# Kernel tuning notes

Measured on AMD Instinct MI355X. Metric: run time of the kernel, lower is better.

The kernel has to match this reference:

```python
import jax, jax.numpy as jnp
import numpy as np

IS, OS, H = 168, 24, 256           # input window, output horizon, state_hsize
TAU, MAXIMUM = 0.1, 1.0            # tau parameter (non-grad) and series maximum
DILS = [[1, 4], [16, 64]]          # ResidualDRNN groups of dilations


def _lstm(x, wih, whh, bih, bhh):
    """Single-layer LSTM over time-major x: (T, B, C). PyTorch gate order i,f,g,o."""
    def step(carry, xt):
        h, c = carry
        g = xt @ wih.T + h @ whh.T + (bih + bhh)
        i, f, gg, o = jnp.split(g, 4, axis=-1)
        c = jax.nn.sigmoid(f) * c + jax.nn.sigmoid(i) * jnp.tanh(gg)
        h = jax.nn.sigmoid(o) * jnp.tanh(c)
        return (h, c), h
    h0 = jnp.zeros((x.shape[1], H), x.dtype)
    _, hs = jax.lax.scan(step, (h0, h0), x)
    return hs


def _dilated_lstm(x, d, p):
    """Standard DRNN layer: pad T to multiple of d, interleave time into batch, run LSTM."""
    T, B, C = x.shape
    n = -(-T // d)
    xp = jnp.pad(x, ((0, n * d - T), (0, 0), (0, 0)))
    hd = _lstm(xp.reshape(n, d * B, C), *p)
    return hd.reshape(n * d, B, H)[:T]


def _forward(train, init_lev_sm, lstm_params, nl_w, nl_b, sc_w, sc_b):
    B, T = train.shape
    a = jax.nn.sigmoid(init_lev_sm[0])            # lev_sms (idxs are all 0 -> same scalar)
    floor = TAU * MAXIMUM                          # tau * maximum
    # --- exponential-smoothing level recurrence (sequential) ---
    lev0 = jnp.maximum(train[:, 0], floor)
    def step(lev, xt):
        new = jnp.maximum(a * xt + (1.0 - a) * lev, floor)
        return new, new
    _, rest = jax.lax.scan(step, lev0, train[:, 1:].T)
    levs = jnp.concatenate([lev0[None], rest], axis=0).T   # [B, T]
    # --- windowed normalization ---
    w_idx = jnp.arange(IS - 1, T)                           # W = T - IS + 1 window ends
    in_win = train[:, (w_idx - IS + 1)[:, None] + jnp.arange(IS)[None, :]]
    in_win = (in_win / levs[:, w_idx][:, :, None]).transpose(1, 0, 2)    # [W, B, IS]
    o_idx = jnp.arange(IS - 1, T - OS)                      # W_out = T - OS - IS + 1
    out_win = train[:, (o_idx + 1)[:, None] + jnp.arange(OS)[None, :]]
    out_win = (out_win / levs[:, o_idx][:, :, None]).transpose(1, 0, 2)  # [W_out, B, OS]
    # --- ResidualDRNN stack on window_input[:-OS] (time-major: windows are the sequence) ---
    x = in_win[:-OS]
    li = 0
    for g, dils in enumerate(DILS):
        residual = x
        h = x
        for d in dils:
            h = _dilated_lstm(h, d, lstm_params[li])
            li += 1
        x = h + residual if g > 0 else h                    # dropout p=0 -> identity
    x = jnp.tanh(x @ nl_w.T + nl_b)                         # add_nl_layer
    pred = x @ sc_w.T + sc_b                                # scoring
    return pred, out_win


def setup_inputs() -> dict:
    key = jax.random.key(0)
    ks = list(jax.random.split(key, 32))
    B, T = 32, 1024
    inp = {
        "train": jax.random.uniform(ks[0], (B, T), jnp.float32, 0.05, 1.0),
        "val": jax.random.uniform(ks[1], (B, T), jnp.float32, 0.05, 1.0),
        "test": jax.random.uniform(ks[2], (B, T), jnp.float32, 0.05, 1.0),
        "idxs": jnp.zeros((B,), jnp.int32),
        "init_lev_sm": jnp.array([0.5], jnp.float32),
    }
    sizes = [IS, H, H, H]  # input feature size of each of the 4 DRNN layers
    k = 3
    s = 1.0 / np.sqrt(H)
    for i, cin in enumerate(sizes):
        inp[f"wih{i}"] = jax.random.uniform(ks[k], (4 * H, cin), jnp.float32, -s, s); k += 1
        inp[f"whh{i}"] = jax.random.uniform(ks[k], (4 * H, H), jnp.float32, -s, s); k += 1
        inp[f"bih{i}"] = jax.random.uniform(ks[k], (4 * H,), jnp.float32, -s, s); k += 1
        inp[f"bhh{i}"] = jax.random.uniform(ks[k], (4 * H,), jnp.float32, -s, s); k += 1
    inp["nl_w"] = jax.random.uniform(ks[k], (H, H), jnp.float32, -s, s); k += 1
    inp["nl_b"] = jnp.zeros((H,), jnp.float32)
    inp["sc_w"] = jax.random.uniform(ks[k], (OS, H), jnp.float32, -s, s); k += 1
    inp["sc_b"] = jnp.zeros((OS,), jnp.float32)
    return inp


def reference(train, val, test, idxs, init_lev_sm,
              wih0, whh0, bih0, bhh0, wih1, whh1, bih1, bhh1,
              wih2, whh2, bih2, bhh2, wih3, whh3, bih3, bhh3,
              nl_w, nl_b, sc_w, sc_b):
    lstm_params = [(wih0, whh0, bih0, bhh0), (wih1, whh1, bih1, bhh1),
                   (wih2, whh2, bih2, bhh2), (wih3, whh3, bih3, bhh3)]
    # training path (validating=False, testing=False): only `train` is used
    return _forward(train, init_lev_sm, lstm_params, nl_w, nl_b, sc_w, sc_b)
```

## Files before the change

kernel.cpp:

```cpp
#include <hip/hip_runtime.h>
#include <hip/hip_fp16.h>
#include <math.h>

#define TT 833
#define GDIM 1024

typedef _Float16 f16x8 __attribute__((ext_vector_type(8)));
typedef float    f32x4 __attribute__((ext_vector_type(4)));

#if __has_builtin(__builtin_amdgcn_rcpf)
__device__ __forceinline__ float frcp(float x){ return __builtin_amdgcn_rcpf(x); }
#else
__device__ __forceinline__ float frcp(float x){ return 1.f/x; }
#endif

#if __has_builtin(__builtin_amdgcn_sdot4)
__device__ __forceinline__ int sdot4(unsigned a, unsigned b, int c){
  return __builtin_amdgcn_sdot4((int)a, (int)b, c, false);
}
#else
__device__ __forceinline__ int sdot4(unsigned a, unsigned b, int c){
  int ai = (int)a, bi = (int)b;
  c += ((ai<<24)>>24)*((bi<<24)>>24);
  c += ((ai<<16)>>24)*((bi<<16)>>24);
  c += ((ai<<8)>>24)*((bi<<8)>>24);
  c += (ai>>24)*(bi>>24);
  return c;
}
#endif

__device__ __forceinline__ void lds_barrier(){
  asm volatile("s_waitcnt lgkmcnt(0)" ::: "memory");
  __builtin_amdgcn_s_barrier();
  __builtin_amdgcn_sched_barrier(0);
}


__global__ void levels_k(const float* __restrict__ train, const float* __restrict__ ism,
                         float* __restrict__ levs){
  int b = threadIdx.x;
  if (b >= 32) return;
  float a = 1.f/(1.f+expf(-ism[0]));
  const float4* tr4 = reinterpret_cast<const float4*>(train + b*1024);
  float4* lv4 = reinterpret_cast<float4*>(levs + b*1024);
  float lev = 0.f;
  for (int i = 0; i < 256; ++i){
    float4 v = tr4[i];
    float4 o;
    if (i == 0) o.x = lev = fmaxf(v.x, 0.1f);
    else        o.x = lev = fmaxf(fmaf(a, v.x, (1.f-a)*lev), 0.1f);
    o.y = lev = fmaxf(fmaf(a, v.y, (1.f-a)*lev), 0.1f);
    o.z = lev = fmaxf(fmaf(a, v.z, (1.f-a)*lev), 0.1f);
    o.w = lev = fmaxf(fmaf(a, v.w, (1.f-a)*lev), 0.1f);
    lv4[i] = o;
  }
}

__global__ void win_x_k(const float* __restrict__ train, const float* __restrict__ levs,
                        __half* __restrict__ x0){
  int idx = blockIdx.x*256 + threadIdx.x;
  int i = idx % 192;
  int r = idx / 192;
  int b = r & 31;
  int t = r >> 5;
  x0[idx] = (i < 168) ? __float2half(train[b*1024 + t + i] / levs[b*1024 + t + 167])
                      : __float2half(0.f);
}

__global__ void win_out_k(const float* __restrict__ train, const float* __restrict__ levs,
                          float* __restrict__ ow){
  int idx = blockIdx.x*256 + threadIdx.x;
  int o = idx % 24;
  int r = idx / 24;
  int b = r & 31;
  int t = r >> 5;
  ow[idx] = train[b*1024 + 168 + t + o] / levs[b*1024 + t + 167];
}

__global__ void permw_k(const float* __restrict__ wih, const float* __restrict__ bih,
                        const float* __restrict__ bhh, __half* __restrict__ wP,
                        float* __restrict__ bP, int K, int Kpad){
  int t = blockIdx.x;
  int g = ((t & 3) << 8) + (t >> 2);
  for (int k = threadIdx.x; k < Kpad; k += 256)
    wP[(size_t)t*Kpad + k] = (k < K) ? __float2half(wih[(size_t)g*K + k]) : __float2half(0.f);
  if (threadIdx.x == 0) bP[t] = bih[g] + bhh[g];
}

__global__ void cvth_k(const float* __restrict__ s, __half* __restrict__ d, int n){
  int i = blockIdx.x*256 + threadIdx.x;
  if (i < n) d[i] = __float2half(s[i]);
}

__global__ void packq_k(const float* __restrict__ w, uint4* __restrict__ wq,
                        float* __restrict__ sc){
  int t = blockIdx.x*256 + threadIdx.x;
  if (t >= 1024) return;
  int g = ((t & 3) << 8) + (t >> 2);
  const float* row = w + (size_t)g*256;
  float amax = 0.f;
  for (int k = 0; k < 256; ++k) amax = fmaxf(amax, fabsf(row[k]));
  amax = fmaxf(amax, 1e-20f);
  float s = amax/127.f, inv = 127.f/amax;
  sc[t] = s;
  for (int k16 = 0; k16 < 16; ++k16){
    union { uint4 u; signed char b[16]; } r;
    #pragma unroll
    for (int j = 0; j < 16; ++j){
      float q = rintf(row[k16*16 + j]*inv);
      q = fminf(fmaxf(q, -127.f), 127.f);
      r.b[j] = (signed char)q;
    }
    wq[(size_t)k16*1024 + t] = r.u;
  }
}

__global__ __launch_bounds__(256) void proj_direct(
    const _Float16* __restrict__ A, const _Float16* __restrict__ W,
    const float* __restrict__ b1,
    void* __restrict__ C, int Mout, int K, int N, int dil, int act, int outHalf)
{
  const int tid = threadIdx.x;
  const int lane = tid & 63;
  const int w = tid >> 6, wr = w >> 1, wc = w & 1;
  const int m0 = blockIdx.y << 7, n0 = blockIdx.x << 7;
  const int kg = lane >> 4, r16 = lane & 15;

  int srow[4];
  #pragma unroll
  for (int mi = 0; mi < 4; ++mi){
    int m = m0 + wr*64 + mi*16 + r16;
    int row;
    if (dil == 0) row = (m < Mout) ? m : -1;
    else {
      int rows = dil << 5;
      int jj = m / rows;
      int q = m - jj*rows;
      int t = jj*dil + (q >> 5);
      row = (t < TT) ? ((t << 5) + (q & 31)) : -1;
    }
    srow[mi] = row;
  }
  const _Float16* wbase[4];
  #pragma unroll
  for (int nj = 0; nj < 4; ++nj)
    wbase[nj] = W + (size_t)(n0 + wc*64 + nj*16 + r16)*K;

  f32x4 acc[4][4];
  #pragma unroll
  for (int i = 0; i < 4; ++i)
    #pragma unroll
    for (int j = 0; j < 4; ++j) acc[i][j] = (f32x4){0.f,0.f,0.f,0.f};

  const int nkt = K >> 5;
  #pragma unroll 2
  for (int kt = 0; kt < nkt; ++kt){
    const int k = (kt << 5) + kg*8;
    f16x8 af[4], bf[4];
    #pragma unroll
    for (int mi = 0; mi < 4; ++mi){
      af[mi] = (f16x8){0,0,0,0,0,0,0,0};
      if (srow[mi] >= 0)
        af[mi] = *reinterpret_cast<const f16x8*>(A + (size_t)srow[mi]*K + k);
    }
    #pragma unroll
    for (int nj = 0; nj < 4; ++nj)
      bf[nj] = *reinterpret_cast<const f16x8*>(wbase[nj] + k);
    #pragma unroll
    for (int mi = 0; mi < 4; ++mi)
      #pragma unroll
      for (int nj = 0; nj < 4; ++nj)
        acc[mi][nj] = __builtin_amdgcn_mfma_f32_16x16x32_f16(af[mi], bf[nj], acc[mi][nj], 0, 0, 0);
  }
  #pragma unroll
  for (int mi = 0; mi < 4; ++mi){
    #pragma unroll
    for (int p = 0; p < 4; ++p){
      int mrow = m0 + wr*64 + mi*16 + (lane >> 4)*4 + p;
      if (mrow >= Mout) continue;
      #pragma unroll
      for (int nj = 0; nj < 4; ++nj){
        int ncol = n0 + wc*64 + nj*16 + (lane & 15);
        float v = acc[mi][nj][p] + b1[ncol];
        if (act) v = tanhf(v);
        if (outHalf) reinterpret_cast<__half*>(C)[(size_t)mrow*N + ncol] = __float2half(v);
        else reinterpret_cast<float*>(C)[(size_t)mrow*N + ncol] = v;
      }
    }
  }
}

template<int NR>
__global__ __launch_bounds__(512, 1) void srecr2_k(
    const uint4* __restrict__ wq, const float* __restrict__ scale,
    const __half* __restrict__ Gin,
    __half* __restrict__ outh, float* __restrict__ outf,
    int nsteps, int d, int rowsTotal)
{
  __shared__ __align__(16) unsigned int hq[2][NR][64];
  const int tid = threadIdx.x;
  const int s = tid & 1;
  const int j = tid >> 1;
  const int q0 = blockIdx.x*NR;
  const float sg0 = scale[2*tid]*(1.f/127.f);
  const float sg1 = scale[2*tid + 1]*(1.f/127.f);
  uint4 w0_[16], w1_[16];
  #pragma unroll
  for (int kk = 0; kk < 16; ++kk){
    w0_[kk] = wq[(size_t)kk*1024 + 2*tid];
    w1_[kk] = wq[(size_t)kk*1024 + 2*tid + 1];
  }
  float c[NR];
  #pragma unroll
  for (int rr = 0; rr < NR; ++rr) c[rr] = 0.f;
  for (int e = tid; e < 2*NR*64; e += 512) (&hq[0][0][0])[e] = 0u;
  __syncthreads();

  for (int step = 0; step < nsteps; ++step){
    const int cur = step & 1;
    const __half2* gbase = reinterpret_cast<const __half2*>(
        Gin + ((size_t)step*rowsTotal + q0)*GDIM);
    #pragma unroll
    for (int rr = 0; rr < NR; ++rr){
      __half2 g2 = gbase[rr*512 + tid];
      float gin0 = __half2float(__low2half(g2));
      float gin1 = __half2float(__high2half(g2));
      int a00 = 0, a01 = 0, a10 = 0, a11 = 0;
      #pragma unroll
      for (int k16 = 0; k16 < 8; ++k16){
        uint4 ha = *reinterpret_cast<const uint4*>(&hq[cur][rr][4*k16]);
        a00 = sdot4(w0_[k16].x, ha.x, a00); a00 = sdot4(w0_[k16].y, ha.y, a00);
        a00 = sdot4(w0_[k16].z, ha.z, a00); a00 = sdot4(w0_[k16].w, ha.w, a00);
        a10 = sdot4(w1_[k16].x, ha.x, a10); a10 = sdot4(w1_[k16].y, ha.y, a10);
        a10 = sdot4(w1_[k16].z, ha.z, a10); a10 = sdot4(w1_[k16].w, ha.w, a10);
        uint4 hb = *reinterpret_cast<const uint4*>(&hq[cur][rr][4*(k16 + 8)]);
        a01 = sdot4(w0_[k16+8].x, hb.x, a01); a01 = sdot4(w0_[k16+8].y, hb.y, a01);
        a01 = sdot4(w0_[k16+8].z, hb.z, a01); a01 = sdot4(w0_[k16+8].w, hb.w, a01);
        a11 = sdot4(w1_[k16+8].x, hb.x, a11); a11 = sdot4(w1_[k16+8].y, hb.y, a11);
        a11 = sdot4(w1_[k16+8].z, hb.z, a11); a11 = sdot4(w1_[k16+8].w, hb.w, a11);
      }
      float p0 = fmaf((float)(a00 + a01), sg0, gin0);
      float p1 = fmaf((float)(a10 + a11), sg1, gin1);
      float px0 = s ? p0 + p0 : p0;
      float t0 = frcp(1.f + __expf(-px0));
      float a0v = s ? fmaf(2.f, t0, -1.f) : t0;
      float a1v = frcp(1.f + __expf(-p1));
      float b0 = __shfl_xor(a0v, 1);
      float b1 = __shfl_xor(a1v, 1);
      float iv = s ? b0 : a0v;
      float fv = s ? b1 : a1v;
      float gv = s ? a0v : b0;
      float ov = s ? a1v : b1;
      float cn = fmaf(fv, c[rr], iv*gv);
      c[rr] = cn;
      if (s == 0){
        float e2 = __expf(-2.f*cn);
        float h = ov*(1.f - e2)*frcp(1.f + e2);
        int qh = (int)rintf(h*127.f);
        reinterpret_cast<signed char*>(&hq[cur^1][rr][0])[j] = (signed char)qh;
        int q = q0 + rr;
        int tg = step*d + (q >> 5);
        if (tg < TT){
          size_t oi = ((size_t)tg*32 + (q & 31))*256 + j;
          outh[oi] = __float2half(h);
          if (outf) outf[oi] = h;
        }
      }
    }
    lds_barrier();
  }
}

template<int NR>
__global__ __launch_bounds__(1024) void srecq_k(
    const uint4* __restrict__ wq, const float* __restrict__ scale,
    const __half* __restrict__ Gin,
    __half* __restrict__ outh, const float* __restrict__ res,
    int nsteps, int d, int rowsTotal)
{
  __shared__ __align__(16) unsigned int hq[2][NR][64];
  const int tid = threadIdx.x;
  const int lane = tid & 63;
  const int base = lane & ~3;
  const int kg = tid & 3;
  const int j = tid >> 2;
  const int q0 = blockIdx.x*NR;
  const float sg = scale[tid]*(1.f/127.f);
  float c[NR];
  #pragma unroll
  for (int rr = 0; rr < NR; ++rr) c[rr] = 0.f;
  for (int e = tid; e < 2*NR*64; e += 1024) (&hq[0][0][0])[e] = 0u;
  __syncthreads();

  for (int step = 0; step < nsteps; ++step){
    const int cur = step & 1;
    float gin[NR];
    const __half* gbase = Gin + ((size_t)step*rowsTotal + q0)*GDIM;
    #pragma unroll
    for (int rr = 0; rr < NR; ++rr) gin[rr] = __half2float(gbase[rr*GDIM + tid]);
    int acc[NR];
    #pragma unroll
    for (int rr = 0; rr < NR; ++rr) acc[rr] = 0;
    #pragma unroll 4
    for (int k16 = 0; k16 < 16; ++k16){
      uint4 w = wq[(size_t)k16*1024 + tid];
      #pragma unroll
      for (int rr = 0; rr < NR; ++rr){
        uint4 h4 = *reinterpret_cast<const uint4*>(&hq[cur][rr][4*k16]);
        acc[rr] = sdot4(w.x, h4.x, acc[rr]);
        acc[rr] = sdot4(w.y, h4.y, acc[rr]);
        acc[rr] = sdot4(w.z, h4.z, acc[rr]);
        acc[rr] = sdot4(w.w, h4.w, acc[rr]);
      }
    }
    #pragma unroll
    for (int rr = 0; rr < NR; ++rr){
      float p = fmaf((float)acc[rr], sg, gin[rr]);
      float px = (kg == 2) ? p + p : p;
      float sv = frcp(1.f + __expf(-px));
      float a = (kg == 2) ? fmaf(2.f, sv, -1.f) : sv;
      float iv = __shfl(a, base + 0);
      float fv = __shfl(a, base + 1);
      float gv = __shfl(a, base + 2);
      float ov = __shfl(a, base + 3);
      float cn = fmaf(fv, c[rr], iv*gv);
      c[rr] = cn;
      float e2 = __expf(-2.f*cn);
      float h = ov*(1.f - e2)*frcp(1.f + e2);
      if (kg == 0){
        int qh = (int)rintf(h*127.f);
        reinterpret_cast<signed char*>(&hq[cur^1][rr][0])[j] = (signed char)qh;
        int q = q0 + rr;
        int tg = step*d + (q >> 5);
        if (tg < TT){
          size_t oi = ((size_t)tg*32 + (q & 31))*256 + j;
          outh[oi] = __float2half(h + res[oi]);
        }
      }
    }
    lds_barrier();
  }
}

__global__ __launch_bounds__(256) void sc_head(const __half* __restrict__ xt, const float* __restrict__ w,
                        const float* __restrict__ bias, float* __restrict__ outp, int M){
  __shared__ float arow[8][256];
  int m0 = blockIdx.x << 3;
  int tid = threadIdx.x;
  #pragma unroll
  for (int i = 0; i < 8; ++i){
    int e = tid + (i << 8);
    int r = e >> 8, k = e & 255;
    arow[r][k] = (m0 + r < M) ? __half2float(xt[(size_t)(m0 + r)*256 + k]) : 0.f;
  }
  __syncthreads();
  int r = tid >> 5, n = tid & 31;
  if (n < 24 && (m0 + r) < M){
    float acc = bias[n];
    const float* wr = w + n*256;
    #pragma unroll 8
    for (int k = 0; k < 256; ++k) acc = fmaf(arow[r][k], wr[k], acc);
    outp[(size_t)(m0 + r)*24 + n] = acc;
  }
}

extern "C" void kernel_launch(void* const* d_in, const int* in_sizes, int n_in,
                              void* d_out, int out_size, void* d_ws, size_t ws_size,
                              hipStream_t stream){
  const float* train = (const float*)d_in[0];
  const float* ism   = (const float*)d_in[4];
  const float* wih[4] = {(const float*)d_in[5], (const float*)d_in[9], (const float*)d_in[13], (const float*)d_in[17]};
  const float* whh[4] = {(const float*)d_in[6], (const float*)d_in[10], (const float*)d_in[14], (const float*)d_in[18]};
  const float* bih[4] = {(const float*)d_in[7], (const float*)d_in[11], (const float*)d_in[15], (const float*)d_in[19]};
  const float* bhh[4] = {(const float*)d_in[8], (const float*)d_in[12], (const float*)d_in[16], (const float*)d_in[20]};
  const float* nl_w = (const float*)d_in[21];
  const float* nl_b = (const float*)d_in[22];
  const float* sc_w = (const float*)d_in[23];
  const float* sc_b = (const float*)d_in[24];
  float* out = (float*)d_out;

  float* ws = (float*)d_ws;
  size_t off = 0;
  float* levs = ws + off;   off += 32768;
  uint4* wqk[4];
  for (int l = 0; l < 4; ++l){ wqk[l] = (uint4*)(ws + off); off += 65536; }
  float* sck[4];
  for (int l = 0; l < 4; ++l){ sck[l] = ws + off; off += 1024; }
  __half* wPh[4];
  for (int l = 0; l < 4; ++l){ wPh[l] = (__half*)(ws + off); off += 131072; }
  float* bP[4];
  for (int l = 0; l < 4; ++l){ bP[l] = ws + off; off += 1024; }
  __half* nlwh = (__half*)(ws + off); off += 32768;
  __half* x0h = (__half*)(ws + off);  off += (size_t)26656*192/2;
  __half* G   = (__half*)(ws + off);  off += (size_t)28672*1024/2;
  __half* h0h = (__half*)(ws + off);  off += (size_t)26656*256/2;
  __half* h1h = (__half*)(ws + off);  off += (size_t)26656*256/2;
  float*  h1f = ws + off;             off += (size_t)26656*256;
  __half* h2h = (__half*)(ws + off);  off += (size_t)26656*256/2;
  __half* xfh = (__half*)(ws + off);  off += (size_t)26656*256/2;
  __half* xth = (__half*)(ws + off);  off += (size_t)26656*256/2;
  (void)ws_size; (void)in_sizes; (void)n_in; (void)out_size;

  levels_k<<<1, 64, 0, stream>>>(train, ism, levs);
  win_x_k<<<19992, 256, 0, stream>>>(train, levs, x0h);
  win_out_k<<<2499, 256, 0, stream>>>(train, levs, out + 639744);
  const int Kin[4]  = {168, 256, 256, 256};
  const int Kpad[4] = {192, 256, 256, 256};
  for (int l = 0; l < 4; ++l){
    packq_k<<<4, 256, 0, stream>>>(whh[l], wqk[l], sck[l]);
    permw_k<<<1024, 256, 0, stream>>>(wih[l], bih[l], bhh[l], wPh[l], bP[l], Kin[l], Kpad[l]);
  }
  cvth_k<<<256, 256, 0, stream>>>(nl_w, nlwh, 65536);

  proj_direct<<<dim3(8,209), 256, 0, stream>>>((const _Float16*)x0h, (const _Float16*)wPh[0], bP[0], G, 26656, 192, 1024, 0, 0, 1);
  srecr2_k<1><<<32, 512, 0, stream>>>(wqk[0], sck[0], G, h0h, nullptr, 833, 1, 32);
  proj_direct<<<dim3(8,209), 256, 0, stream>>>((const _Float16*)h0h, (const _Float16*)wPh[1], bP[1], G, 26752, 256, 1024, 4, 0, 1);
  srecr2_k<1><<<128, 512, 0, stream>>>(wqk[1], sck[1], G, h1h, h1f, 209, 4, 128);
  proj_direct<<<dim3(8,212), 256, 0, stream>>>((const _Float16*)h1h, (const _Float16*)wPh[2], bP[2], G, 27136, 256, 1024, 16, 0, 1);
  srecr2_k<2><<<256, 512, 0, stream>>>(wqk[2], sck[2], G, h2h, nullptr, 53, 16, 512);
  proj_direct<<<dim3(8,224), 256, 0, stream>>>((const _Float16*)h2h, (const _Float16*)wPh[3], bP[3], G, 28672, 256, 1024, 64, 0, 1);
  srecq_k<8><<<256, 1024, 0, stream>>>(wqk[3], sck[3], G, xfh, h1f, 14, 64, 2048);
  proj_direct<<<dim3(2,209), 256, 0, stream>>>((const _Float16*)xfh, (const _Float16*)nlwh, nl_b, xth, 26656, 256, 256, 0, 1, 1);
  sc_head<<<3332, 256, 0, stream>>>(xth, sc_w, sc_b, out, 26656);
}
```

Baseline: 1.761 ms.

## Stage projection GEMM tiles through LDS with 256x128 blocks of 512 threads

The input projection GEMM now stages the A and B tiles into padded shared memory each k-step, with 8 waves per block covering a 256x128 output tile, instead of each wave loading its MFMA fragments straight from global memory. The aim is to share the loaded tiles across waves and use coalesced global loads, which cuts redundant global traffic. In exchange it adds two barriers per k-iteration with no double buffering, and larger blocks, which may limit overlap. An unrelated reorder of two sdot4 calls in the recurrence kernel is also included.

```diff
diff --git a/kernel.cpp b/kernel.cpp
--- a/kernel.cpp
+++ b/kernel.cpp
@@ -115,36 +115,34 @@
   }
 }
 
-__global__ __launch_bounds__(256) void proj_direct(
+__global__ __launch_bounds__(512) void proj_mfma(
     const _Float16* __restrict__ A, const _Float16* __restrict__ W,
     const float* __restrict__ b1,
     void* __restrict__ C, int Mout, int K, int N, int dil, int act, int outHalf)
 {
+  __shared__ _Float16 As[256*40];
+  __shared__ _Float16 Bs[128*40];
   const int tid = threadIdx.x;
   const int lane = tid & 63;
   const int w = tid >> 6, wr = w >> 1, wc = w & 1;
-  const int m0 = blockIdx.y << 7, n0 = blockIdx.x << 7;
-  const int kg = lane >> 4, r16 = lane & 15;
-
-  int srow[4];
-  #pragma unroll
-  for (int mi = 0; mi < 4; ++mi){
-    int m = m0 + wr*64 + mi*16 + r16;
-    int row;
-    if (dil == 0) row = (m < Mout) ? m : -1;
+  const int m0 = blockIdx.y << 8, n0 = blockIdx.x << 7;
+
+  const int rowA = tid >> 1;
+  const int halfsel = tid & 1;
+  int srcrow;
+  {
+    int m = m0 + rowA;
+    if (dil == 0) srcrow = (m < Mout) ? m : -1;
     else {
       int rows = dil << 5;
       int jj = m / rows;
       int q = m - jj*rows;
       int t = jj*dil + (q >> 5);
-      row = (t < TT) ? ((t << 5) + (q & 31)) : -1;
-    }
-    srow[mi] = row;
-  }
-  const _Float16* wbase[4];
-  #pragma unroll
-  for (int nj = 0; nj < 4; ++nj)
-    wbase[nj] = W + (size_t)(n0 + wc*64 + nj*16 + r16)*K;
+      srcrow = (t < TT) ? ((t << 5) + (q & 31)) : -1;
+    }
+  }
+  const int rowB = (tid & 255) >> 1;
+  const int nrow = n0 + rowB;
 
   f32x4 acc[4][4];
   #pragma unroll
@@ -153,24 +151,41 @@
     for (int j = 0; j < 4; ++j) acc[i][j] = (f32x4){0.f,0.f,0.f,0.f};
 
   const int nkt = K >> 5;
-  #pragma unroll 2
   for (int kt = 0; kt < nkt; ++kt){
-    const int k = (kt << 5) + kg*8;
-    f16x8 af[4], bf[4];
-    #pragma unroll
-    for (int mi = 0; mi < 4; ++mi){
-      af[mi] = (f16x8){0,0,0,0,0,0,0,0};
-      if (srow[mi] >= 0)
-        af[mi] = *reinterpret_cast<const f16x8*>(A + (size_t)srow[mi]*K + k);
-    }
-    #pragma unroll
-    for (int nj = 0; nj < 4; ++nj)
-      bf[nj] = *reinterpret_cast<const f16x8*>(wbase[nj] + k);
-    #pragma unroll
-    for (int mi = 0; mi < 4; ++mi)
+    const int k0 = (kt << 5) + halfsel*16;
+    {
+      union { uint4 u[2]; _Float16 h[16]; } tmp;
+      if (srcrow >= 0){
+        const uint4* s = reinterpret_cast<const uint4*>(A + (size_t)srcrow*K + k0);
+        tmp.u[0] = s[0]; tmp.u[1] = s[1];
+      } else {
+        tmp.u[0] = make_uint4(0,0,0,0); tmp.u[1] = make_uint4(0,0,0,0);
+      }
+      uint4* dst = reinterpret_cast<uint4*>(&As[rowA*40 + halfsel*16]);
+      dst[0] = tmp.u[0]; dst[1] = tmp.u[1];
+    }
+    if (tid < 256){
+      const uint4* s = reinterpret_cast<const uint4*>(W + (size_t)nrow*K + k0);
+      uint4* dst = reinterpret_cast<uint4*>(&Bs[rowB*40 + halfsel*16]);
+      dst[0] = s[0]; dst[1] = s[1];
+    }
+    __syncthreads();
+    {
+      const int kg = lane >> 4, r16 = lane & 15;
+      f16x8 af[4], bf[4];
+      #pragma unroll
+      for (int mi = 0; mi < 4; ++mi)
+        af[mi] = *reinterpret_cast<const f16x8*>(&As[(wr*64 + mi*16 + r16)*40 + kg*8]);
       #pragma unroll
       for (int nj = 0; nj < 4; ++nj)
-        acc[mi][nj] = __builtin_amdgcn_mfma_f32_16x16x32_f16(af[mi], bf[nj], acc[mi][nj], 0, 0, 0);
+        bf[nj] = *reinterpret_cast<const f16x8*>(&Bs[(wc*64 + nj*16 + r16)*40 + kg*8]);
+      #pragma unroll
+      for (int mi = 0; mi < 4; ++mi)
+        #pragma unroll
+        for (int nj = 0; nj < 4; ++nj)
+          acc[mi][nj] = __builtin_amdgcn_mfma_f32_16x16x32_f16(af[mi], bf[nj], acc[mi][nj], 0, 0, 0);
+    }
+    __syncthreads();
   }
   #pragma unroll
   for (int mi = 0; mi < 4; ++mi){
@@ -237,7 +252,7 @@
         a01 = sdot4(w0_[k16+8].x, hb.x, a01); a01 = sdot4(w0_[k16+8].y, hb.y, a01);
         a01 = sdot4(w0_[k16+8].z, hb.z, a01); a01 = sdot4(w0_[k16+8].w, hb.w, a01);
         a11 = sdot4(w1_[k16+8].x, hb.x, a11); a11 = sdot4(w1_[k16+8].y, hb.y, a11);
-        a11 = sdot4(w1_[k16+8].z, hb.z, a11); a11 = sdot4(w1_[k16+8].w, hb.w, a11);
+        a11 = sdot4(w1_[k16+8].w, hb.w, a11); a11 = sdot4(w1_[k16+8].z, hb.z, a11);
       }
       float p0 = fmaf((float)(a00 + a01), sg0, gin0);
       float p1 = fmaf((float)(a10 + a11), sg1, gin1);
@@ -412,14 +427,14 @@
   }
   cvth_k<<<256, 256, 0, stream>>>(nl_w, nlwh, 65536);
 
-  proj_direct<<<dim3(8,209), 256, 0, stream>>>((const _Float16*)x0h, (const _Float16*)wPh[0], bP[0], G, 26656, 192, 1024, 0, 0, 1);
+  proj_mfma<<<dim3(8,105), 512, 0, stream>>>((const _Float16*)x0h, (const _Float16*)wPh[0], bP[0], G, 26656, 192, 1024, 0, 0, 1);
   srecr2_k<1><<<32, 512, 0, stream>>>(wqk[0], sck[0], G, h0h, nullptr, 833, 1, 32);
-  proj_direct<<<dim3(8,209), 256, 0, stream>>>((const _Float16*)h0h, (const _Float16*)wPh[1], bP[1], G, 26752, 256, 1024, 4, 0, 1);
+  proj_mfma<<<dim3(8,105), 512, 0, stream>>>((const _Float16*)h0h, (const _Float16*)wPh[1], bP[1], G, 26752, 256, 1024, 4, 0, 1);
   srecr2_k<1><<<128, 512, 0, stream>>>(wqk[1], sck[1], G, h1h, h1f, 209, 4, 128);
-  proj_direct<<<dim3(8,212), 256, 0, stream>>>((const _Float16*)h1h, (const _Float16*)wPh[2], bP[2], G, 27136, 256, 1024, 16, 0, 1);
+  proj_mfma<<<dim3(8,106), 512, 0, stream>>>((const _Float16*)h1h, (const _Float16*)wPh[2], bP[2], G, 27136, 256, 1024, 16, 0, 1);
   srecr2_k<2><<<256, 512, 0, stream>>>(wqk[2], sck[2], G, h2h, nullptr, 53, 16, 512);
-  proj_direct<<<dim3(8,224), 256, 0, stream>>>((const _Float16*)h2h, (const _Float16*)wPh[3], bP[3], G, 28672, 256, 1024, 64, 0, 1);
+  proj_mfma<<<dim3(8,112), 512, 0, stream>>>((const _Float16*)h2h, (const _Float16*)wPh[3], bP[3], G, 28672, 256, 1024, 64, 0, 1);
   srecq_k<8><<<256, 1024, 0, stream>>>(wqk[3], sck[3], G, xfh, h1f, 14, 64, 2048);
-  proj_direct<<<dim3(2,209), 256, 0, stream>>>((const _Float16*)xfh, (const _Float16*)nlwh, nl_b, xth, 26656, 256, 256, 0, 1, 1);
+  proj_mfma<<<dim3(2,105), 512, 0, stream>>>((const _Float16*)xfh, (const _Float16*)nlwh, nl_b, xth, 26656, 256, 256, 0, 1, 1);
   sc_head<<<3332, 256, 0, stream>>>(xth, sc_w, sc_b, out, 26656);
 }
```

New measurement: 1.613 ms. -8.4%, faster.
